# Performance work log

Measured on AMD Instinct MI355X. Metric: run time of the kernel, lower is better.

## Reference

```python
import jax, jax.numpy as jnp
import numpy as np
import math

B, T, D, K, KER, H = 2, 2048, 1024, 16, 7, 2048


def _decay_logit_init(k: int, dmin: float = 0.9, dmax: float = 0.999) -> np.ndarray:
    decays = np.exp(np.linspace(math.log(dmin), math.log(dmax), k))
    return (np.log(decays) - np.log1p(-decays)).astype(np.float32)


def setup_inputs() -> dict:
    key = jax.random.key(0)
    ks = jax.random.split(key, 12)
    s = 0.02
    return {
        "x": jax.random.normal(ks[0], (B, T, D), jnp.float32),
        "conv_w": jax.random.normal(ks[1], (D, KER), jnp.float32) * s,   # depthwise causal conv taps
        "gate_w": jax.random.normal(ks[2], (D, D), jnp.float32) * (D ** -0.5),
        "gate_b": jnp.zeros((D,), jnp.float32),
        "up_w": jax.random.normal(ks[3], (D, H), jnp.float32) * (D ** -0.5),
        "up_b": jnp.zeros((H,), jnp.float32),
        "down_w": jax.random.normal(ks[4], (H, D), jnp.float32) * (H ** -0.5),
        "down_b": jnp.zeros((D,), jnp.float32),
        "sin_w": jax.random.normal(ks[5], (D, K * D), jnp.float32) * (D ** -0.5),
        "sout_w": jax.random.normal(ks[6], (K * D, D), jnp.float32) * ((K * D) ** -0.5),
        "decay_logit": jnp.asarray(_decay_logit_init(K)),
        "gl_w": jax.random.normal(ks[7], (D, 1), jnp.float32) * (D ** -0.5),
        "gl_b": jnp.zeros((1,), jnp.float32),
    }


def _rmsnorm(x, eps=1e-6):
    return x * jax.lax.rsqrt(jnp.mean(x * x, axis=-1, keepdims=True) + eps)


def reference(x, conv_w, gate_w, gate_b, up_w, up_b, down_w, down_b,
              sin_w, sout_w, decay_logit, gl_w, gl_b):
    b, t, d = x.shape
    k_taps = conv_w.shape[1]
    nk = decay_logit.shape[0]

    u = _rmsnorm(x)  # (B,T,D)

    # --- local mixer: causal depthwise conv (zero history buffer) + sigmoid gate + SiLU MLP ---
    u_pad = jnp.pad(u, ((0, 0), (k_taps - 1, 0), (0, 0)))
    y = sum(conv_w[:, j] * u_pad[:, j:j + t, :] for j in range(k_taps))  # (B,T,D)
    g = jax.nn.sigmoid(u @ gate_w + gate_b)
    h = y * g
    local = jax.nn.silu(h @ up_w + up_b) @ down_w + down_b

    # --- state bank: K leaky integrators, s_t = a*s_{t-1} + (1-a)*z_t ---
    z = (u @ sin_w).reshape(b, t, nk, d)  # (B,T,K,D)
    a = jax.nn.sigmoid(decay_logit)[:, None]  # (K,1)

    def step(s, z_t):
        s = a * s + (1.0 - a) * z_t
        return s, s

    s0 = jnp.zeros((b, nk, d), x.dtype)
    _, S = jax.lax.scan(step, s0, jnp.swapaxes(z, 0, 1))  # (T,B,K,D)
    S = jnp.swapaxes(S, 0, 1).reshape(b, t, nk * d)
    long_path = S @ sout_w  # (B,T,D)

    # --- gate fusion + residual (memory table is empty at init -> mem term == 0) ---
    g_long = jax.nn.sigmoid(u @ gl_w + gl_b)  # (B,T,1)
    return x + local + g_long * long_path
```

## Files before the change

kernel.cpp:

```cpp
#include <hip/hip_runtime.h>
#include <cstdint>
#include <cstddef>

typedef __attribute__((ext_vector_type(8))) short short8;
typedef __attribute__((ext_vector_type(4))) float floatx4;

#define DEV static __device__ __forceinline__

#define PSTRIDE ((size_t)4096 * 1024)

DEV unsigned short f2bf(float f) {
  union { float f; uint32_t u; } v; v.f = f;
  uint32_t r = v.u + 0x7fffu + ((v.u >> 16) & 1u);
  return (unsigned short)(r >> 16);
}
DEV float bf2f(unsigned short h) {
  union { uint32_t u; float f; } v; v.u = ((uint32_t)h) << 16; return v.f;
}
DEV float sigmoidf_(float x) { return 1.f / (1.f + __expf(-x)); }

DEV void gld_lds16(const unsigned short* g, unsigned short* l) {
  __builtin_amdgcn_global_load_lds(
      (const __attribute__((address_space(1))) void*)g,
      (__attribute__((address_space(3))) void*)l, 16, 0, 0);
}

__global__ __launch_bounds__(256) void transpose_kernel(
    const float* __restrict__ W, unsigned short* __restrict__ Wt,
    int Kdim, int Ndim) {
  __shared__ float tile[32][33];
  const int n0 = blockIdx.x * 32;
  const int k0 = blockIdx.y * 32;
  const int tx = threadIdx.x & 31;
  const int ty = threadIdx.x >> 5;
#pragma unroll
  for (int r = 0; r < 32; r += 8)
    tile[ty + r][tx] = W[(size_t)(k0 + ty + r) * Ndim + n0 + tx];
  __syncthreads();
#pragma unroll
  for (int r = 0; r < 32; r += 8)
    Wt[(size_t)(n0 + ty + r) * Kdim + k0 + tx] = f2bf(tile[tx][ty + r]);
}

__global__ __launch_bounds__(256) void cast_kernel(
    const float* __restrict__ W, unsigned short* __restrict__ Wb) {
  const size_t i = (size_t)blockIdx.x * 256 + threadIdx.x;
  const float4 v = ((const float4*)W)[i];
  ushort4 o;
  o.x = f2bf(v.x); o.y = f2bf(v.y); o.z = f2bf(v.z); o.w = f2bf(v.w);
  ((ushort4*)Wb)[i] = o;
}

__global__ __launch_bounds__(256) void rmsnorm_kernel(
    const float* __restrict__ x, const float* __restrict__ gl_w,
    const float* __restrict__ gl_b, unsigned short* __restrict__ u,
    float* __restrict__ gl_logit) {
  const int row = blockIdx.x;
  const int tid = threadIdx.x;
  const float4 v = ((const float4*)(x + (size_t)row * 1024))[tid];
  float ss = v.x * v.x + v.y * v.y + v.z * v.z + v.w * v.w;
#pragma unroll
  for (int o = 32; o > 0; o >>= 1) ss += __shfl_down(ss, o, 64);
  __shared__ float red[4];
  if ((tid & 63) == 0) red[tid >> 6] = ss;
  __syncthreads();
  const float tot = red[0] + red[1] + red[2] + red[3];
  const float r = rsqrtf(tot * (1.f / 1024.f) + 1e-6f);
  const float ux = v.x * r, uy = v.y * r, uz = v.z * r, uw = v.w * r;
  ushort4 ub;
  ub.x = f2bf(ux); ub.y = f2bf(uy); ub.z = f2bf(uz); ub.w = f2bf(uw);
  ((ushort4*)(u + (size_t)row * 1024))[tid] = ub;
  const float4 w4 = ((const float4*)gl_w)[tid];
  float dot = ux * w4.x + uy * w4.y + uz * w4.z + uw * w4.w;
#pragma unroll
  for (int o = 32; o > 0; o >>= 1) dot += __shfl_down(dot, o, 64);
  __syncthreads();
  if ((tid & 63) == 0) red[tid >> 6] = dot;
  __syncthreads();
  if (tid == 0) gl_logit[row] = red[0] + red[1] + red[2] + red[3] + gl_b[0];
}

template <int EPI>
__global__ __launch_bounds__(256, 2) void gemm_bt(
    const unsigned short* __restrict__ A, const unsigned short* __restrict__ Bt,
    const float* __restrict__ bias, void* __restrict__ Cout, int Ndim, int Kdim) {
  __shared__ unsigned short As[128 * 32];
  __shared__ unsigned short Bs[128 * 32];
  const int tid = threadIdx.x;
  const int wave = tid >> 6;
  const int lane = tid & 63;
  const size_t row0 = (size_t)blockIdx.x * 128;
  const size_t col0 = (size_t)blockIdx.y * 128;

  const int srow = wave * 32 + (lane >> 2);
  const int kofs = (lane & 3) * 8;
  const unsigned short* pA0 = A + (row0 + srow) * (size_t)Kdim + kofs;
  const unsigned short* pA1 = A + (row0 + srow + 16) * (size_t)Kdim + kofs;
  const unsigned short* pB0 = Bt + (col0 + srow) * (size_t)Kdim + kofs;
  const unsigned short* pB1 = Bt + (col0 + srow + 16) * (size_t)Kdim + kofs;
  unsigned short* lA0 = &As[(wave * 2 + 0) * 512];
  unsigned short* lA1 = &As[(wave * 2 + 1) * 512];
  unsigned short* lB0 = &Bs[(wave * 2 + 0) * 512];
  unsigned short* lB1 = &Bs[(wave * 2 + 1) * 512];

  const int wm = (wave & 1) * 64;
  const int wn = (wave >> 1) * 64;
  const int lr = lane & 15;
  const int lq = lane >> 4;
  const int a_off = (wm + lr) * 32 + lq * 8;
  const int b_off = (wn + lr) * 32 + lq * 8;

  floatx4 acc[4][4];
#pragma unroll
  for (int i = 0; i < 4; i++)
#pragma unroll
    for (int j = 0; j < 4; j++) acc[i][j] = floatx4{0.f, 0.f, 0.f, 0.f};

  for (int kt = 0; kt < Kdim; kt += 32) {
    __syncthreads();
    gld_lds16(pA0, lA0);
    gld_lds16(pA1, lA1);
    gld_lds16(pB0, lB0);
    gld_lds16(pB1, lB1);
    pA0 += 32; pA1 += 32; pB0 += 32; pB1 += 32;
    __syncthreads();
    short8 af[4], bfr[4];
#pragma unroll
    for (int i = 0; i < 4; i++) af[i] = *(const short8*)&As[a_off + i * 16 * 32];
#pragma unroll
    for (int j = 0; j < 4; j++) bfr[j] = *(const short8*)&Bs[b_off + j * 16 * 32];
#pragma unroll
    for (int i = 0; i < 4; i++)
#pragma unroll
      for (int j = 0; j < 4; j++)
        acc[i][j] = __builtin_amdgcn_mfma_f32_16x16x32_bf16(af[i], bfr[j], acc[i][j], 0, 0, 0);
  }

#pragma unroll
  for (int i = 0; i < 4; i++) {
    const size_t rbase = row0 + wm + 16 * i + lq * 4;
#pragma unroll
    for (int j = 0; j < 4; j++) {
      const size_t c = col0 + wn + 16 * j + lr;
#pragma unroll
      for (int r = 0; r < 4; r++) {
        float v = acc[i][j][r];
        const size_t off = (rbase + r) * (size_t)Ndim + c;
        if constexpr (EPI == 2) {
          v += bias[c];
          ((unsigned short*)Cout)[off] = f2bf(v * sigmoidf_(v));
        } else {
          ((unsigned short*)Cout)[off] = f2bf(v);
        }
      }
    }
  }
}

__global__ __launch_bounds__(256, 2) void gemm_splitkP(
    const unsigned short* __restrict__ A, const unsigned short* __restrict__ Bt,
    unsigned short* __restrict__ PBase, int Kdim, int splitLen) {
  __shared__ unsigned short As[128 * 32];
  __shared__ unsigned short Bs[128 * 32];
  const int split = blockIdx.z;
  const int k0 = split * splitLen;
  const int klen = min(splitLen, Kdim - k0);
  const int tid = threadIdx.x;
  const int wave = tid >> 6;
  const int lane = tid & 63;
  const size_t row0 = (size_t)blockIdx.x * 128;
  const size_t col0 = (size_t)blockIdx.y * 128;

  const int srow = wave * 32 + (lane >> 2);
  const int kofs = (lane & 3) * 8;
  const unsigned short* pA0 = A + (row0 + srow) * (size_t)Kdim + k0 + kofs;
  const unsigned short* pA1 = A + (row0 + srow + 16) * (size_t)Kdim + k0 + kofs;
  const unsigned short* pB0 = Bt + (col0 + srow) * (size_t)Kdim + k0 + kofs;
  const unsigned short* pB1 = Bt + (col0 + srow + 16) * (size_t)Kdim + k0 + kofs;
  unsigned short* lA0 = &As[(wave * 2 + 0) * 512];
  unsigned short* lA1 = &As[(wave * 2 + 1) * 512];
  unsigned short* lB0 = &Bs[(wave * 2 + 0) * 512];
  unsigned short* lB1 = &Bs[(wave * 2 + 1) * 512];

  const int wm = (wave & 1) * 64;
  const int wn = (wave >> 1) * 64;
  const int lr = lane & 15;
  const int lq = lane >> 4;
  const int a_off = (wm + lr) * 32 + lq * 8;
  const int b_off = (wn + lr) * 32 + lq * 8;

  floatx4 acc[4][4];
#pragma unroll
  for (int i = 0; i < 4; i++)
#pragma unroll
    for (int j = 0; j < 4; j++) acc[i][j] = floatx4{0.f, 0.f, 0.f, 0.f};

  for (int kt = 0; kt < klen; kt += 32) {
    __syncthreads();
    gld_lds16(pA0, lA0);
    gld_lds16(pA1, lA1);
    gld_lds16(pB0, lB0);
    gld_lds16(pB1, lB1);
    pA0 += 32; pA1 += 32; pB0 += 32; pB1 += 32;
    __syncthreads();
    short8 af[4], bfr[4];
#pragma unroll
    for (int i = 0; i < 4; i++) af[i] = *(const short8*)&As[a_off + i * 16 * 32];
#pragma unroll
    for (int j = 0; j < 4; j++) bfr[j] = *(const short8*)&Bs[b_off + j * 16 * 32];
#pragma unroll
    for (int i = 0; i < 4; i++)
#pragma unroll
      for (int j = 0; j < 4; j++)
        acc[i][j] = __builtin_amdgcn_mfma_f32_16x16x32_bf16(af[i], bfr[j], acc[i][j], 0, 0, 0);
  }

  unsigned short* P = PBase + (size_t)split * PSTRIDE;
#pragma unroll
  for (int i = 0; i < 4; i++) {
    const size_t rbase = row0 + wm + 16 * i + lq * 4;
#pragma unroll
    for (int j = 0; j < 4; j++) {
      const size_t c = col0 + wn + 16 * j + lr;
#pragma unroll
      for (int r = 0; r < 4; r++)
        P[(rbase + r) * 1024 + c] = f2bf(acc[i][j][r]);
    }
  }
}

template <int MODE>
__global__ __launch_bounds__(512, 2) void gemm256(
    const unsigned short* __restrict__ A, const unsigned short* __restrict__ B,
    unsigned short* __restrict__ Cbase, int splitLen) {
  __shared__ unsigned short lds[65536];
  constexpr int LD = (MODE == 2) ? 2048 : 16384;
  const int tid = threadIdx.x;
  const int w = tid >> 6;
  const int l = tid & 63;
  const int wr = w >> 2;
  const int wc = w & 3;
  const size_t row0 = (size_t)blockIdx.x * 256;
  const size_t col0 = (size_t)blockIdx.y * 256;
  const int z = blockIdx.z;
  int k0, nkt;
  if constexpr (MODE == 0) {
    k0 = z * splitLen;
    int klen = 16384 - k0; if (klen > splitLen) klen = splitLen;
    nkt = klen >> 6;
  } else if constexpr (MODE == 1) {
    k0 = z << 10; nkt = 16;
  } else {
    k0 = z << 9; nkt = 8;
  }

  const int lrow = l >> 3;
  const int lcol = (l & 7) ^ lrow;
  const unsigned short* gA = A + (row0 + w * 16 + lrow) * (size_t)LD + k0 + lcol * 8;
  const unsigned short* gB = B + (col0 + w * 16 + lrow) * (size_t)LD + k0 + lcol * 8;
  const int sA = w * 1024;
  const int sB = 16384 + w * 1024;

  const int lr = l & 15;
  const int lq = l >> 4;
  const int aoff = (wr * 128 + lr) * 64 + ((lq ^ (lr & 7)) * 8);
  const int boff = 16384 + (wc * 64 + lr) * 64 + ((lq ^ (lr & 7)) * 8);

#define STG_A(bufb, st, h) { \
    const unsigned short* s_ = gA + (size_t)(h) * (128 * LD) + (size_t)(st) * 64; \
    unsigned short* d_ = &lds[(bufb) * 32768 + (h) * 8192 + sA]; \
    gld_lds16(s_, d_); gld_lds16(s_ + 8 * LD, d_ + 512); }
#define STG_B(bufb, st, h) { \
    const unsigned short* s_ = gB + (size_t)(h) * (128 * LD) + (size_t)(st) * 64; \
    unsigned short* d_ = &lds[(bufb) * 32768 + (h) * 8192 + sB]; \
    gld_lds16(s_, d_); gld_lds16(s_ + 8 * LD, d_ + 512); }

  floatx4 acc[8][4];
#pragma unroll
  for (int i = 0; i < 8; ++i)
#pragma unroll
    for (int j = 0; j < 4; ++j) acc[i][j] = floatx4{0.f, 0.f, 0.f, 0.f};

  STG_A(0, 0, 0) STG_A(0, 0, 1) STG_B(0, 0, 0) STG_B(0, 0, 1)
  STG_B(1, 1, 0) STG_B(1, 1, 1)
  asm volatile("s_waitcnt vmcnt(4)" ::: "memory");
  __builtin_amdgcn_s_barrier();

  short8 bfr[4][2];

#define MM2(MI, NJ) \
  acc[MI][NJ] = __builtin_amdgcn_mfma_f32_16x16x32_bf16(af_[(MI) & 1][0], bfr[NJ][0], acc[MI][NJ], 0, 0, 0); \
  acc[MI][NJ] = __builtin_amdgcn_mfma_f32_16x16x32_bf16(af_[(MI) & 1][1], bfr[NJ][1], acc[MI][NJ], 0, 0, 0);

#define PHASE(Q, STAGE_STMT, TAIL) { \
    short8 af_[2][2]; \
    af_[0][0] = *(const short8*)&lds[cb + aoff + (Q * 2 + 0) * 1024]; \
    af_[0][1] = *(const short8*)&lds[cb + (aoff ^ 32) + (Q * 2 + 0) * 1024]; \
    af_[1][0] = *(const short8*)&lds[cb + aoff + (Q * 2 + 1) * 1024]; \
    af_[1][1] = *(const short8*)&lds[cb + (aoff ^ 32) + (Q * 2 + 1) * 1024]; \
    STAGE_STMT \
    __builtin_amdgcn_s_barrier(); \
    asm volatile("s_waitcnt lgkmcnt(0)" ::: "memory"); \
    __builtin_amdgcn_sched_barrier(0); \
    __builtin_amdgcn_s_setprio(1); \
    MM2(Q * 2 + 0, 0) MM2(Q * 2 + 0, 1) MM2(Q * 2 + 0, 2) MM2(Q * 2 + 0, 3) \
    MM2(Q * 2 + 1, 0) MM2(Q * 2 + 1, 1) MM2(Q * 2 + 1, 2) MM2(Q * 2 + 1, 3) \
    __builtin_amdgcn_s_setprio(0); \
    TAIL; \
    __builtin_amdgcn_s_barrier(); }

  for (int S = 0; S < nkt; ++S) {
    const int cur = S & 1;
    const int oth = cur ^ 1;
    const int cb = cur * 32768;
    const int t1 = (S + 1 < nkt) ? S + 1 : nkt - 1;
    const int t2 = (S + 2 < nkt) ? S + 2 : nkt - 1;
#pragma unroll
    for (int nj = 0; nj < 4; ++nj) {
      bfr[nj][0] = *(const short8*)&lds[cb + boff + nj * 1024];
      bfr[nj][1] = *(const short8*)&lds[cb + (boff ^ 32) + nj * 1024];
    }
    PHASE(0, STG_A(oth, t1, 0), )
    PHASE(1, STG_A(oth, t1, 1), )
    PHASE(2, STG_B(cur, t2, 0), )
    PHASE(3, STG_B(cur, t2, 1), asm volatile("s_waitcnt vmcnt(4)" ::: "memory"))
  }

#pragma unroll
  for (int mi = 0; mi < 8; ++mi) {
    const size_t r0 = row0 + wr * 128 + mi * 16 + lq * 4;
#pragma unroll
    for (int nj = 0; nj < 4; ++nj) {
      const size_t c = col0 + wc * 64 + nj * 16 + lr;
#pragma unroll
      for (int r = 0; r < 4; ++r) {
        const float v = acc[mi][nj][r];
        if constexpr (MODE == 1)
          Cbase[(r0 + r) * 16384 + ((size_t)z << 10) + c] = f2bf(v);
        else
          Cbase[(size_t)z * PSTRIDE + (r0 + r) * 1024 + c] = f2bf(v);
      }
    }
  }
#undef PHASE
#undef MM2
#undef STG_A
#undef STG_B
}

__global__ __launch_bounds__(256) void convgate2_kernel(
    const unsigned short* __restrict__ u, const float* __restrict__ conv_w,
    const unsigned short* __restrict__ gp, const float* __restrict__ gate_b,
    unsigned short* __restrict__ h) {
  const size_t idx = (size_t)blockIdx.x * 256 + threadIdx.x;
  const int d = (int)(idx & 1023);
  const int t = (int)((idx >> 10) & 2047);
  const unsigned short* up = u + idx;
  float acc = 0.f;
#pragma unroll
  for (int j = 0; j < 7; ++j) {
    const int tt = t - 6 + j;
    if (tt >= 0) acc += conv_w[d * 7 + j] * bf2f(up[(j - 6) * 1024]);
  }
  const float logit = bf2f(gp[idx]) + bf2f(gp[idx + PSTRIDE]) + gate_b[d];
  h[idx] = f2bf(acc * sigmoidf_(logit));
}

__global__ __launch_bounds__(256) void fold4_kernel(
    const float* __restrict__ x, const unsigned short* __restrict__ dp,
    const float* __restrict__ down_b, float* __restrict__ out) {
  const size_t idx = (size_t)blockIdx.x * 256 + threadIdx.x;
  const float s = bf2f(dp[idx]) + bf2f(dp[idx + PSTRIDE]) +
                  bf2f(dp[idx + 2 * PSTRIDE]) + bf2f(dp[idx + 3 * PSTRIDE]);
  out[idx] = x[idx] + s + down_b[idx & 1023];
}

template <int NS>
__global__ __launch_bounds__(256) void reduceNg_kernel(
    const unsigned short* __restrict__ p, const float* __restrict__ gl,
    float* __restrict__ out) {
  const size_t idx = (size_t)blockIdx.x * 256 + threadIdx.x;
  const float g = sigmoidf_(gl[idx >> 10]);
  float s = 0.f;
#pragma unroll
  for (int i = 0; i < NS; ++i) s += bf2f(p[idx + (size_t)i * PSTRIDE]);
  out[idx] += g * s;
}

__global__ __launch_bounds__(256) void scan1u_kernel(
    const unsigned short* __restrict__ u, const float* __restrict__ decay_logit,
    float* __restrict__ carry) {
  const int gid = blockIdx.x * 256 + threadIdx.x;
  const int d = gid & 1023;
  const int b = (gid >> 10) & 1;
  const int c = gid >> 11;
  float a[16], s[16];
#pragma unroll
  for (int k = 0; k < 16; ++k) { a[k] = sigmoidf_(decay_logit[k]); s[k] = 0.f; }
  const unsigned short* p = u + ((size_t)b * 2048 + c * 128) * 1024 + d;
#pragma unroll 2
  for (int t = 0; t < 128; ++t) {
    const float uv = bf2f(*p);
    p += 1024;
#pragma unroll
    for (int k = 0; k < 16; ++k) s[k] = fmaf(a[k], s[k], (1.f - a[k]) * uv);
  }
#pragma unroll
  for (int k = 0; k < 16; ++k)
    carry[(size_t)((c * 2 + b) * 16 + k) * 1024 + d] = s[k];
}

__global__ __launch_bounds__(256) void scan2u_kernel(
    float* __restrict__ carry, const float* __restrict__ decay_logit) {
  const int gid = blockIdx.x * 256 + threadIdx.x;
  const int d = gid & 1023;
  const int k = (gid >> 10) & 15;
  const int b = gid >> 14;
  const float a = sigmoidf_(decay_logit[k]);
  float aL = a;
#pragma unroll
  for (int i = 0; i < 7; ++i) aL *= aL;
  float s = 0.f;
#pragma unroll
  for (int c = 0; c < 16; ++c) {
    const size_t idx = (size_t)((c * 2 + b) * 16 + k) * 1024 + d;
    const float Lc = carry[idx];
    carry[idx] = s;
    s = fmaf(aL, s, Lc);
  }
}

__global__ __launch_bounds__(256) void scan3u_kernel(
    const unsigned short* __restrict__ u, const float* __restrict__ decay_logit,
    const float* __restrict__ carry, unsigned short* __restrict__ Ucat) {
  const int gid = blockIdx.x * 256 + threadIdx.x;
  const int d = gid & 1023;
  const int k = (gid >> 10) & 15;
  const int b = (gid >> 14) & 1;
  const int c = gid >> 15;
  const float a = sigmoidf_(decay_logit[k]);
  const float na = 1.f - a;
  float s = carry[(size_t)((c * 2 + b) * 16 + k) * 1024 + d];
  const unsigned short* p = u + ((size_t)b * 2048 + c * 128) * 1024 + d;
  unsigned short* q = Ucat + ((size_t)b * 2048 + c * 128) * 16384 + k * 1024 + d;
#pragma unroll 4
  for (int t = 0; t < 128; ++t) {
    s = fmaf(a, s, na * bf2f(*p));
    *q = f2bf(s);
    p += 1024;
    q += 16384;
  }
}

extern "C" void kernel_launch(void* const* d_in, const int* in_sizes, int n_in,
                              void* d_out, int out_size, void* d_ws,
                              size_t ws_size, hipStream_t stream) {
  const float* x      = (const float*)d_in[0];
  const float* conv_w = (const float*)d_in[1];
  const float* gate_w = (const float*)d_in[2];
  const float* gate_b = (const float*)d_in[3];
  const float* up_w   = (const float*)d_in[4];
  const float* up_b   = (const float*)d_in[5];
  const float* down_w = (const float*)d_in[6];
  const float* down_b = (const float*)d_in[7];
  const float* sin_w  = (const float*)d_in[8];
  const float* sout_w = (const float*)d_in[9];
  const float* decay  = (const float*)d_in[10];
  const float* gl_w   = (const float*)d_in[11];
  const float* gl_b   = (const float*)d_in[12];
  float* out = (float*)d_out;
  char* ws = (char*)d_ws;

  const bool big = ws_size >= (((size_t)192 << 20) + ((size_t)1 << 16));

  auto Ucat = (unsigned short*)(ws + ((size_t)0 << 20));
  auto GWT  = (unsigned short*)(ws + ((size_t)0 << 20));
  auto GP   = (unsigned short*)(ws + ((size_t)2 << 20));
  auto Hb   = (unsigned short*)(ws + ((size_t)18 << 20));
  auto UWT  = (unsigned short*)(ws + ((size_t)26 << 20));
  auto Mb   = (unsigned short*)(ws + ((size_t)30 << 20));
  auto DWT  = (unsigned short*)(ws + ((size_t)46 << 20));
  auto DP   = (unsigned short*)(ws + ((size_t)50 << 20));
  auto SB   = (unsigned short*)(ws + ((size_t)0 << 20));
  auto OT   = (unsigned short*)(ws + ((size_t)32 << 20));
  auto MT   = (unsigned short*)(ws + ((size_t)128 << 20));
  auto U    = (unsigned short*)(ws + ((size_t)160 << 20));
  auto P    = (unsigned short*)(ws + ((size_t)160 << 20));
  auto CARRY= (float*)(ws + ((size_t)168 << 20));
  auto GL   = (float*)(ws + (big ? ((size_t)192 << 20) : ((size_t)184 << 20)));

  rmsnorm_kernel<<<4096, 256, 0, stream>>>(x, gl_w, gl_b, U, GL);

  transpose_kernel<<<dim3(32, 32), 256, 0, stream>>>(gate_w, GWT, 1024, 1024);
  gemm_splitkP<<<dim3(32, 8, 2), 256, 0, stream>>>(U, GWT, GP, 1024, 512);
  convgate2_kernel<<<16384, 256, 0, stream>>>(U, conv_w, GP, gate_b, Hb);
  transpose_kernel<<<dim3(64, 32), 256, 0, stream>>>(up_w, UWT, 1024, 2048);
  gemm_bt<2><<<dim3(32, 16), 256, 0, stream>>>(Hb, UWT, up_b, Mb, 2048, 1024);
  transpose_kernel<<<dim3(32, 64), 256, 0, stream>>>(down_w, DWT, 2048, 1024);
  gemm256<2><<<dim3(16, 4, 4), 512, 0, stream>>>(Mb, DWT, DP, 512);
  fold4_kernel<<<16384, 256, 0, stream>>>(x, DP, down_b, out);

  cast_kernel<<<16384, 256, 0, stream>>>(sin_w, SB);
  transpose_kernel<<<dim3(32, 512), 256, 0, stream>>>(sout_w, OT, 16384, 1024);
  gemm256<1><<<dim3(4, 4, 16), 512, 0, stream>>>(OT, SB, MT, 1024);

  scan1u_kernel<<<128, 256, 0, stream>>>(U, decay, CARRY);
  scan2u_kernel<<<128, 256, 0, stream>>>(CARRY, decay);
  scan3u_kernel<<<2048, 256, 0, stream>>>(U, decay, CARRY, Ucat);

  if (big) {
    gemm256<0><<<dim3(16, 4, 4), 512, 0, stream>>>(Ucat, MT, P, 4096);
    reduceNg_kernel<4><<<16384, 256, 0, stream>>>(P, GL, out);
  } else {
    gemm256<0><<<dim3(16, 4, 3), 512, 0, stream>>>(Ucat, MT, P, 5504);
    reduceNg_kernel<3><<<16384, 256, 0, stream>>>(P, GL, out);
  }
}
```

Before: 533.4 us.

## Software-pipeline A-fragment LDS reads across MFMA phases with partial lgkmcnt waits

Restructures the GEMM inner loop so the next phase's A fragments are loaded from LDS into a second register set while the current phase's MFMAs run. Waits drop from lgkmcnt(0) to partial counts, so the first phase can start issuing MFMAs as each B fragment arrives. The aim is to hide LDS read latency behind matrix-core work. It costs extra fragment registers and depends on the exact lgkmcnt counts matching the order in which loads are issued; a wrong count would consume stale data.

```diff
diff --git a/kernel.cpp b/kernel.cpp
--- a/kernel.cpp
+++ b/kernel.cpp
@@ -287,27 +287,25 @@
   __builtin_amdgcn_s_barrier();
 
   short8 bfr[4][2];
-
-#define MM2(MI, NJ) \
-  acc[MI][NJ] = __builtin_amdgcn_mfma_f32_16x16x32_bf16(af_[(MI) & 1][0], bfr[NJ][0], acc[MI][NJ], 0, 0, 0); \
-  acc[MI][NJ] = __builtin_amdgcn_mfma_f32_16x16x32_bf16(af_[(MI) & 1][1], bfr[NJ][1], acc[MI][NJ], 0, 0, 0);
-
-#define PHASE(Q, STAGE_STMT, TAIL) { \
-    short8 af_[2][2]; \
-    af_[0][0] = *(const short8*)&lds[cb + aoff + (Q * 2 + 0) * 1024]; \
-    af_[0][1] = *(const short8*)&lds[cb + (aoff ^ 32) + (Q * 2 + 0) * 1024]; \
-    af_[1][0] = *(const short8*)&lds[cb + aoff + (Q * 2 + 1) * 1024]; \
-    af_[1][1] = *(const short8*)&lds[cb + (aoff ^ 32) + (Q * 2 + 1) * 1024]; \
-    STAGE_STMT \
-    __builtin_amdgcn_s_barrier(); \
-    asm volatile("s_waitcnt lgkmcnt(0)" ::: "memory"); \
-    __builtin_amdgcn_sched_barrier(0); \
-    __builtin_amdgcn_s_setprio(1); \
-    MM2(Q * 2 + 0, 0) MM2(Q * 2 + 0, 1) MM2(Q * 2 + 0, 2) MM2(Q * 2 + 0, 3) \
-    MM2(Q * 2 + 1, 0) MM2(Q * 2 + 1, 1) MM2(Q * 2 + 1, 2) MM2(Q * 2 + 1, 3) \
-    __builtin_amdgcn_s_setprio(0); \
-    TAIL; \
-    __builtin_amdgcn_s_barrier(); }
+  short8 afA[2][2], afB[2][2];
+
+#define LD_AF(DST, MI) \
+    DST[0][0] = *(const short8*)&lds[cb + aoff + (MI) * 1024]; \
+    DST[0][1] = *(const short8*)&lds[cb + (aoff ^ 32) + (MI) * 1024]; \
+    DST[1][0] = *(const short8*)&lds[cb + aoff + ((MI) + 1) * 1024]; \
+    DST[1][1] = *(const short8*)&lds[cb + (aoff ^ 32) + ((MI) + 1) * 1024];
+
+#define MM2(AF, IP, AR, NJ) \
+  acc[AR][NJ] = __builtin_amdgcn_mfma_f32_16x16x32_bf16(AF[IP][0], bfr[NJ][0], acc[AR][NJ], 0, 0, 0); \
+  acc[AR][NJ] = __builtin_amdgcn_mfma_f32_16x16x32_bf16(AF[IP][1], bfr[NJ][1], acc[AR][NJ], 0, 0, 0);
+
+#define MFMA16(AF, AR0) \
+  MM2(AF, 0, AR0, 0) MM2(AF, 0, AR0, 1) MM2(AF, 0, AR0, 2) MM2(AF, 0, AR0, 3) \
+  MM2(AF, 1, (AR0) + 1, 0) MM2(AF, 1, (AR0) + 1, 1) MM2(AF, 1, (AR0) + 1, 2) MM2(AF, 1, (AR0) + 1, 3)
+
+#define LGKM_SB(N) \
+  asm volatile("s_waitcnt lgkmcnt(" #N ")" ::: "memory"); \
+  __builtin_amdgcn_sched_barrier(0);
 
   for (int S = 0; S < nkt; ++S) {
     const int cur = S & 1;
@@ -315,15 +313,51 @@
     const int cb = cur * 32768;
     const int t1 = (S + 1 < nkt) ? S + 1 : nkt - 1;
     const int t2 = (S + 2 < nkt) ? S + 2 : nkt - 1;
+
+    LD_AF(afA, 0)
 #pragma unroll
     for (int nj = 0; nj < 4; ++nj) {
       bfr[nj][0] = *(const short8*)&lds[cb + boff + nj * 1024];
       bfr[nj][1] = *(const short8*)&lds[cb + (boff ^ 32) + nj * 1024];
     }
-    PHASE(0, STG_A(oth, t1, 0), )
-    PHASE(1, STG_A(oth, t1, 1), )
-    PHASE(2, STG_B(cur, t2, 0), )
-    PHASE(3, STG_B(cur, t2, 1), asm volatile("s_waitcnt vmcnt(4)" ::: "memory"))
+    STG_A(oth, t1, 0)
+    LD_AF(afB, 2)
+    __builtin_amdgcn_s_barrier();
+    __builtin_amdgcn_s_setprio(1);
+    LGKM_SB(10)
+    MM2(afA, 0, 0, 0) MM2(afA, 1, 1, 0)
+    LGKM_SB(8)
+    MM2(afA, 0, 0, 1) MM2(afA, 1, 1, 1)
+    LGKM_SB(6)
+    MM2(afA, 0, 0, 2) MM2(afA, 1, 1, 2)
+    LGKM_SB(4)
+    MM2(afA, 0, 0, 3) MM2(afA, 1, 1, 3)
+    __builtin_amdgcn_s_setprio(0);
+    __builtin_amdgcn_s_barrier();
+    STG_A(oth, t1, 1)
+    LD_AF(afA, 4)
+    __builtin_amdgcn_s_barrier();
+    __builtin_amdgcn_s_setprio(1);
+    LGKM_SB(4)
+    MFMA16(afB, 2)
+    __builtin_amdgcn_s_setprio(0);
+    __builtin_amdgcn_s_barrier();
+    STG_B(cur, t2, 0)
+    LD_AF(afB, 6)
+    __builtin_amdgcn_s_barrier();
+    __builtin_amdgcn_s_setprio(1);
+    LGKM_SB(4)
+    MFMA16(afA, 4)
+    __builtin_amdgcn_s_setprio(0);
+    __builtin_amdgcn_s_barrier();
+    STG_B(cur, t2, 1)
+    __builtin_amdgcn_s_barrier();
+    __builtin_amdgcn_s_setprio(1);
+    LGKM_SB(0)
+    MFMA16(afB, 6)
+    __builtin_amdgcn_s_setprio(0);
+    asm volatile("s_waitcnt vmcnt(4)" ::: "memory");
+    __builtin_amdgcn_s_barrier();
   }
 
 #pragma unroll
@@ -342,8 +376,10 @@
       }
     }
   }
-#undef PHASE
+#undef LGKM_SB
+#undef MFMA16
 #undef MM2
+#undef LD_AF
 #undef STG_A
 #undef STG_B
 }
```

Result: no change. 527.7 us (-1.1%).

## Fuse causal conv and sigmoid gate into gate GEMM epilogue; interleave MFMA order

Applied to the files above, without the earlier changes.

Replaces the split-K gate GEMM and the separate conv-gate kernel with a single full-K GEMM. Its epilogue computes the depthwise causal conv from U, adds the gate bias, applies the sigmoid and writes h directly. This removes the bf16 partial-sum round trip through memory and one kernel launch, but halves the grid and adds strided reads in the epilogue. Separately, the MFMA issue order in gemm256 is interleaved so that consecutive MFMAs target independent accumulators, which avoids dependency stalls.

```diff
diff --git a/kernel.cpp b/kernel.cpp
--- a/kernel.cpp
+++ b/kernel.cpp
@@ -157,26 +157,25 @@
   }
 }
 
-__global__ __launch_bounds__(256, 2) void gemm_splitkP(
+__global__ __launch_bounds__(256, 2) void gemm_gate(
     const unsigned short* __restrict__ A, const unsigned short* __restrict__ Bt,
-    unsigned short* __restrict__ PBase, int Kdim, int splitLen) {
+    const float* __restrict__ gate_b, const float* __restrict__ conv_w,
+    unsigned short* __restrict__ h) {
   __shared__ unsigned short As[128 * 32];
   __shared__ unsigned short Bs[128 * 32];
-  const int split = blockIdx.z;
-  const int k0 = split * splitLen;
-  const int klen = min(splitLen, Kdim - k0);
   const int tid = threadIdx.x;
   const int wave = tid >> 6;
   const int lane = tid & 63;
   const size_t row0 = (size_t)blockIdx.x * 128;
   const size_t col0 = (size_t)blockIdx.y * 128;
+  const int Kdim = 1024;
 
   const int srow = wave * 32 + (lane >> 2);
   const int kofs = (lane & 3) * 8;
-  const unsigned short* pA0 = A + (row0 + srow) * (size_t)Kdim + k0 + kofs;
-  const unsigned short* pA1 = A + (row0 + srow + 16) * (size_t)Kdim + k0 + kofs;
-  const unsigned short* pB0 = Bt + (col0 + srow) * (size_t)Kdim + k0 + kofs;
-  const unsigned short* pB1 = Bt + (col0 + srow + 16) * (size_t)Kdim + k0 + kofs;
+  const unsigned short* pA0 = A + (row0 + srow) * (size_t)Kdim + kofs;
+  const unsigned short* pA1 = A + (row0 + srow + 16) * (size_t)Kdim + kofs;
+  const unsigned short* pB0 = Bt + (col0 + srow) * (size_t)Kdim + kofs;
+  const unsigned short* pB1 = Bt + (col0 + srow + 16) * (size_t)Kdim + kofs;
   unsigned short* lA0 = &As[(wave * 2 + 0) * 512];
   unsigned short* lA1 = &As[(wave * 2 + 1) * 512];
   unsigned short* lB0 = &Bs[(wave * 2 + 0) * 512];
@@ -195,7 +194,7 @@
 #pragma unroll
     for (int j = 0; j < 4; j++) acc[i][j] = floatx4{0.f, 0.f, 0.f, 0.f};
 
-  for (int kt = 0; kt < klen; kt += 32) {
+  for (int kt = 0; kt < Kdim; kt += 32) {
     __syncthreads();
     gld_lds16(pA0, lA0);
     gld_lds16(pA1, lA1);
@@ -215,16 +214,30 @@
         acc[i][j] = __builtin_amdgcn_mfma_f32_16x16x32_bf16(af[i], bfr[j], acc[i][j], 0, 0, 0);
   }
 
-  unsigned short* P = PBase + (size_t)split * PSTRIDE;
 #pragma unroll
   for (int i = 0; i < 4; i++) {
     const size_t rbase = row0 + wm + 16 * i + lq * 4;
 #pragma unroll
     for (int j = 0; j < 4; j++) {
       const size_t c = col0 + wn + 16 * j + lr;
-#pragma unroll
-      for (int r = 0; r < 4; r++)
-        P[(rbase + r) * 1024 + c] = f2bf(acc[i][j][r]);
+      const float gb = gate_b[c];
+      float cw[7];
+#pragma unroll
+      for (int jj = 0; jj < 7; ++jj) cw[jj] = conv_w[c * 7 + jj];
+#pragma unroll
+      for (int r = 0; r < 4; r++) {
+        const size_t row = rbase + r;
+        const int t = (int)(row & 2047);
+        const unsigned short* up = A + row * 1024 + c;
+        float conv = 0.f;
+#pragma unroll
+        for (int jj = 0; jj < 7; ++jj) {
+          const int tt = t - 6 + jj;
+          if (tt >= 0) conv += cw[jj] * bf2f(up[(jj - 6) * 1024]);
+        }
+        const float logit = acc[i][j][r] + gb;
+        h[row * 1024 + c] = f2bf(conv * sigmoidf_(logit));
+      }
     }
   }
 }
@@ -288,9 +301,8 @@
 
   short8 bfr[4][2];
 
-#define MM2(MI, NJ) \
-  acc[MI][NJ] = __builtin_amdgcn_mfma_f32_16x16x32_bf16(af_[(MI) & 1][0], bfr[NJ][0], acc[MI][NJ], 0, 0, 0); \
-  acc[MI][NJ] = __builtin_amdgcn_mfma_f32_16x16x32_bf16(af_[(MI) & 1][1], bfr[NJ][1], acc[MI][NJ], 0, 0, 0);
+#define MM1(IP, AR, NJ, KK) \
+  acc[AR][NJ] = __builtin_amdgcn_mfma_f32_16x16x32_bf16(af_[IP][KK], bfr[NJ][KK], acc[AR][NJ], 0, 0, 0);
 
 #define PHASE(Q, STAGE_STMT, TAIL) { \
     short8 af_[2][2]; \
@@ -303,8 +315,14 @@
     asm volatile("s_waitcnt lgkmcnt(0)" ::: "memory"); \
     __builtin_amdgcn_sched_barrier(0); \
     __builtin_amdgcn_s_setprio(1); \
-    MM2(Q * 2 + 0, 0) MM2(Q * 2 + 0, 1) MM2(Q * 2 + 0, 2) MM2(Q * 2 + 0, 3) \
-    MM2(Q * 2 + 1, 0) MM2(Q * 2 + 1, 1) MM2(Q * 2 + 1, 2) MM2(Q * 2 + 1, 3) \
+    MM1(0, Q * 2 + 0, 0, 0) MM1(1, Q * 2 + 1, 0, 0) \
+    MM1(0, Q * 2 + 0, 1, 0) MM1(1, Q * 2 + 1, 1, 0) \
+    MM1(0, Q * 2 + 0, 2, 0) MM1(1, Q * 2 + 1, 2, 0) \
+    MM1(0, Q * 2 + 0, 3, 0) MM1(1, Q * 2 + 1, 3, 0) \
+    MM1(0, Q * 2 + 0, 0, 1) MM1(1, Q * 2 + 1, 0, 1) \
+    MM1(0, Q * 2 + 0, 1, 1) MM1(1, Q * 2 + 1, 1, 1) \
+    MM1(0, Q * 2 + 0, 2, 1) MM1(1, Q * 2 + 1, 2, 1) \
+    MM1(0, Q * 2 + 0, 3, 1) MM1(1, Q * 2 + 1, 3, 1) \
     __builtin_amdgcn_s_setprio(0); \
     TAIL; \
     __builtin_amdgcn_s_barrier(); }
@@ -343,27 +361,9 @@
     }
   }
 #undef PHASE
-#undef MM2
+#undef MM1
 #undef STG_A
 #undef STG_B
-}
-
-__global__ __launch_bounds__(256) void convgate2_kernel(
-    const unsigned short* __restrict__ u, const float* __restrict__ conv_w,
-    const unsigned short* __restrict__ gp, const float* __restrict__ gate_b,
-    unsigned short* __restrict__ h) {
-  const size_t idx = (size_t)blockIdx.x * 256 + threadIdx.x;
-  const int d = (int)(idx & 1023);
-  const int t = (int)((idx >> 10) & 2047);
-  const unsigned short* up = u + idx;
-  float acc = 0.f;
-#pragma unroll
-  for (int j = 0; j < 7; ++j) {
-    const int tt = t - 6 + j;
-    if (tt >= 0) acc += conv_w[d * 7 + j] * bf2f(up[(j - 6) * 1024]);
-  }
-  const float logit = bf2f(gp[idx]) + bf2f(gp[idx + PSTRIDE]) + gate_b[d];
-  h[idx] = f2bf(acc * sigmoidf_(logit));
 }
 
 __global__ __launch_bounds__(256) void fold4_kernel(
@@ -475,7 +475,6 @@
 
   auto Ucat = (unsigned short*)(ws + ((size_t)0 << 20));
   auto GWT  = (unsigned short*)(ws + ((size_t)0 << 20));
-  auto GP   = (unsigned short*)(ws + ((size_t)2 << 20));
   auto Hb   = (unsigned short*)(ws + ((size_t)18 << 20));
   auto UWT  = (unsigned short*)(ws + ((size_t)26 << 20));
   auto Mb   = (unsigned short*)(ws + ((size_t)30 << 20));
@@ -492,8 +491,7 @@
   rmsnorm_kernel<<<4096, 256, 0, stream>>>(x, gl_w, gl_b, U, GL);
 
   transpose_kernel<<<dim3(32, 32), 256, 0, stream>>>(gate_w, GWT, 1024, 1024);
-  gemm_splitkP<<<dim3(32, 8, 2), 256, 0, stream>>>(U, GWT, GP, 1024, 512);
-  convgate2_kernel<<<16384, 256, 0, stream>>>(U, conv_w, GP, gate_b, Hb);
+  gemm_gate<<<dim3(32, 8), 256, 0, stream>>>(U, GWT, gate_b, conv_w, Hb);
   transpose_kernel<<<dim3(64, 32), 256, 0, stream>>>(up_w, UWT, 1024, 2048);
   gemm_bt<2><<<dim3(32, 16), 256, 0, stream>>>(Hb, UWT, up_b, Mb, 2048, 1024);
   transpose_kernel<<<dim3(32, 64), 256, 0, stream>>>(down_w, DWT, 2048, 1024);
```

Result: no change. 532.7 us (-0.1%).
